# Kernel tuning notes

Hardware: AMD Instinct MI355X
Metric: run time of the kernel (lower is better)

The kernel has to match this reference:

```python
import jax, jax.numpy as jnp
import numpy as np

N_NODES = 50000
N_EDGES = 800000
D_IN = 128
D_OUT = 128


def setup_inputs() -> dict:
    key = jax.random.key(0)
    k1, k2, k3, k4, k5 = jax.random.split(key, 5)
    x = jax.random.normal(k1, (N_NODES, D_IN), dtype=jnp.float32)
    weight = jax.random.normal(k2, (D_IN, D_OUT), dtype=jnp.float32)
    bias = jax.random.normal(k3, (D_OUT,), dtype=jnp.float32)
    vals = jax.random.uniform(k4, (N_EDGES,), dtype=jnp.float32)
    row = jax.random.randint(k5, (N_EDGES,), 0, N_NODES, dtype=jnp.int32)
    col = jax.random.randint(jax.random.fold_in(k5, 1), (N_EDGES,), 0, N_NODES, dtype=jnp.int32)
    return {"x": x, "weight": weight, "bias": bias, "vals": vals, "row": row, "col": col}


def reference(x, weight, bias, vals, row, col):
    # Dense feature transform: x @ W   [N, D_out]
    h = x @ weight
    # SpMM: out[i] = sum_{e: row[e]==i} vals[e] * h[col[e]]
    msg = vals[:, None] * h[col]  # [E, D_out]
    out = jax.ops.segment_sum(msg, row, num_segments=N_NODES)
    # Fused bias + ReLU (original: out += bias; relu(out))
    out = jax.nn.relu(out + bias)
    return out
```

## Files before the change

kernel.cpp:

```cpp
#include <hip/hip_runtime.h>

#define N_NODES 50000
#define N_EDGES 800000
#define D 128
#define D4 32

#define BIN_LOG 6
#define BIN_ROWS 64
#define NBINS ((N_NODES + BIN_ROWS - 1) / BIN_ROWS)
#define CAP 1280

#define NKEYS 512

#define EPB 4096
#define NCHUNK ((N_EDGES + EPB - 1) / EPB)
#define GEMM_BLOCKS ((N_NODES + 63) / 64)
#define E4 (N_EDGES / 4)

#define CAP_CELL 24
#define CELLS_PER_BIN (NCHUNK * CAP_CELL)
#define CNTROW 784

typedef __attribute__((ext_vector_type(8))) short bf16x8;
typedef __attribute__((ext_vector_type(4))) float f32x4;

__device__ __forceinline__ unsigned bf16_1(float a) {
    unsigned u = __float_as_uint(a);
    return (u + 0x7fffu + ((u >> 16) & 1u)) >> 16;
}
__device__ __forceinline__ unsigned pack_bf16(float a, float b) {
    return bf16_1(a) | (bf16_1(b) << 16);
}
__device__ __forceinline__ float ubf_lo(unsigned u) {
    return __uint_as_float(u << 16);
}
__device__ __forceinline__ float ubf_hi(unsigned u) {
    return __uint_as_float(u & 0xffff0000u);
}

__global__ __launch_bounds__(256) void prep_wt(const float* __restrict__ w,
                                               unsigned* __restrict__ wtu) {
    const int i = blockIdx.x * 256 + threadIdx.x;
    if (i < D * 64) {
        const int col = i >> 6;
        const int k2  = i & 63;
        wtu[i] = pack_bf16(w[(size_t)(2 * k2) * D + col],
                           w[(size_t)(2 * k2 + 1) * D + col]);
    }
}

__global__ __launch_bounds__(256) void fused_partition_gemm(
        const float4* __restrict__ x4, const uint4* __restrict__ wt4,
        ushort* __restrict__ hb,
        const int4* __restrict__ rowi4, const int4* __restrict__ coli4,
        const float4* __restrict__ vals4,
        uint2* __restrict__ cells, ushort* __restrict__ cnt_t) {

    if (blockIdx.x < NCHUNK) {
        __shared__ int cur[NBINS];
        const int tid = threadIdx.x;
        for (int i = tid; i < NBINS; i += 256) cur[i] = 0;
        __syncthreads();

        union { int4 v4[4]; int a[16]; } R, C;
        union { float4 v4[4]; float a[16]; } V;
        const int base4 = blockIdx.x * (EPB / 4);
        #pragma unroll
        for (int q = 0; q < 4; ++q) {
            const int i4  = base4 + q * 256 + tid;
            const int i4c = (i4 < E4) ? i4 : (E4 - 1);
            R.v4[q] = rowi4[i4c];
            C.v4[q] = coli4[i4c];
            V.v4[q] = vals4[i4c];
            if (i4 >= E4) R.v4[q] = make_int4(-1, -1, -1, -1);
        }

        #pragma unroll
        for (int q = 0; q < 16; ++q) {
            const int r = R.a[q];
            if (r >= 0) {
                const int b = r >> BIN_LOG;
                const int k = atomicAdd(&cur[b], 1);
                const unsigned c = (unsigned)C.a[q];
                if (k < CAP_CELL)
                    cells[((size_t)b * NCHUNK + blockIdx.x) * CAP_CELL + k] =
                        make_uint2((c << 16) | bf16_1(V.a[q]),
                                   ((unsigned)(r & (BIN_ROWS - 1)) << 3) | (c >> 13));
            }
        }
        __syncthreads();

        ushort* ct = cnt_t + (size_t)blockIdx.x * CNTROW;
        for (int i = tid; i < NBINS; i += 256)
            ct[i] = (ushort)min(cur[i], CAP_CELL);
        return;
    }

    const int bid  = blockIdx.x - NCHUNK;
    const int lane = threadIdx.x & 63;
    const int r0   = bid * 64 + (threadIdx.x >> 6) * 16;
    const int arow = r0 + (lane & 15);
    const int kg   = lane >> 4;
    const bool rok = (arow < N_NODES);

    bf16x8 afr[4];
    #pragma unroll
    for (int kc = 0; kc < 4; ++kc) {
        float4 f0 = make_float4(0.f, 0.f, 0.f, 0.f);
        float4 f1 = f0;
        if (rok) {
            const int c4 = kc * 8 + kg * 2;
            f0 = x4[(size_t)arow * D4 + c4];
            f1 = x4[(size_t)arow * D4 + c4 + 1];
        }
        union { bf16x8 v; unsigned u[4]; } a;
        a.u[0] = pack_bf16(f0.x, f0.y);
        a.u[1] = pack_bf16(f0.z, f0.w);
        a.u[2] = pack_bf16(f1.x, f1.y);
        a.u[3] = pack_bf16(f1.z, f1.w);
        afr[kc] = a.v;
    }

    f32x4 acc[8];
    #pragma unroll
    for (int t = 0; t < 8; ++t) acc[t] = (f32x4){0.f, 0.f, 0.f, 0.f};

    #pragma unroll
    for (int t = 0; t < 8; ++t) {
        const int col = t * 16 + (lane & 15);
        #pragma unroll
        for (int kc = 0; kc < 4; ++kc) {
            union { bf16x8 v; uint4 u; } b;
            b.u = wt4[(size_t)col * 16 + kc * 4 + kg];
            acc[t] = __builtin_amdgcn_mfma_f32_16x16x32_bf16(afr[kc], b.v,
                                                             acc[t], 0, 0, 0);
        }
    }

    #pragma unroll
    for (int t = 0; t < 8; ++t) {
        const int col = t * 16 + (lane & 15);
        #pragma unroll
        for (int j = 0; j < 4; ++j) {
            const int r = r0 + (lane >> 4) * 4 + j;
            if (r < N_NODES)
                hb[(size_t)r * D + col] = (ushort)bf16_1(acc[t][j]);
        }
    }
}

__global__ __launch_bounds__(512) void sort_gather(const ushort* __restrict__ cnt_t,
                                                   const uint2* __restrict__ cells,
                                                   const uint2* __restrict__ hb2,
                                                   const float4* __restrict__ bias4,
                                                   float4* __restrict__ out4) {
    __shared__ ushort   cnt_c[NCHUNK];
    __shared__ int      hcnt[NKEYS];
    __shared__ int      cur[NKEYS];
    __shared__ int      starts[NKEYS + 1];
    __shared__ int      wsum[8], woff[8];
    __shared__ unsigned sorted[CAP];

    const int bin = blockIdx.x;
    const int tid = threadIdx.x;
    const uint2* stripe = cells + (size_t)bin * CELLS_PER_BIN;

    if (tid < NCHUNK) cnt_c[tid] = cnt_t[(size_t)tid * CNTROW + bin];
    if (tid < NKEYS) { hcnt[tid] = 0; cur[tid] = 0; }
    __syncthreads();

    for (int i = tid; i < CELLS_PER_BIN; i += 512) {
        const int c = i / CAP_CELL;
        const int s = i - c * CAP_CELL;
        if (s < (int)cnt_c[c])
            atomicAdd(&hcnt[stripe[i].y & (NKEYS - 1)], 1);
    }
    __syncthreads();

    {
        int v = hcnt[tid];
        #pragma unroll
        for (int off = 1; off < 64; off <<= 1) {
            const int t = __shfl_up(v, off);
            if ((tid & 63) >= off) v += t;
        }
        starts[tid + 1] = v;
        if ((tid & 63) == 63) wsum[tid >> 6] = v;
    }
    __syncthreads();
    if (tid == 0) {
        int run = 0;
        #pragma unroll
        for (int w2 = 0; w2 < 8; ++w2) { woff[w2] = run; run += wsum[w2]; }
        starts[0] = 0;
    }
    __syncthreads();
    starts[tid + 1] += woff[tid >> 6];
    __syncthreads();

    for (int i = tid; i < CELLS_PER_BIN; i += 512) {
        const int c = i / CAP_CELL;
        const int s = i - c * CAP_CELL;
        if (s < (int)cnt_c[c]) {
            const uint2 r = stripe[i];
            const int key = r.y & (NKEYS - 1);
            const int p = atomicAdd(&cur[key], 1);
            const int dst = starts[key] + p;
            if (dst < CAP) sorted[dst] = r.x;
        }
    }
    __syncthreads();

    const int wave = tid >> 6;
    const int lane = tid & 63;
    const int half = lane >> 5;
    const int hl   = lane & 31;
    const float4 b = bias4[hl];

    #pragma unroll
    for (int rp = 0; rp < 4; ++rp) {
        const int row  = wave + 16 * rp + 8 * half;
        const int node = bin * BIN_ROWS + row;
        int s = 0, len = 0;
        if (node < N_NODES) {
            s   = starts[row << 3];
            len = starts[(row << 3) + 8] - s;
        }
        int lm = len;
        lm = max(lm, __shfl_xor(lm, 32));

        float4 acc = {0.f, 0.f, 0.f, 0.f};
        for (int j0 = 0; j0 < lm; j0 += 8) {
            uint2 hv[8];
            float vv[8];
            #pragma unroll
            for (int q = 0; q < 8; ++q) {
                const int jq = j0 + q;
                const int jj = (jq < len) ? (s + jq) : 0;
                unsigned ed = sorted[jj];
                ed = (jq < len) ? ed : 0u;
                vv[q] = __uint_as_float((ed & 0xffffu) << 16);
                hv[q] = hb2[(size_t)(ed >> 16) * 32 + hl];
            }
            #pragma unroll
            for (int q = 0; q < 8; ++q) {
                acc.x = fmaf(vv[q], ubf_lo(hv[q].x), acc.x);
                acc.y = fmaf(vv[q], ubf_hi(hv[q].x), acc.y);
                acc.z = fmaf(vv[q], ubf_lo(hv[q].y), acc.z);
                acc.w = fmaf(vv[q], ubf_hi(hv[q].y), acc.w);
            }
        }
        if (node < N_NODES) {
            float4 o;
            o.x = fmaxf(acc.x + b.x, 0.f);
            o.y = fmaxf(acc.y + b.y, 0.f);
            o.z = fmaxf(acc.z + b.z, 0.f);
            o.w = fmaxf(acc.w + b.w, 0.f);
            out4[(size_t)node * 32 + hl] = o;
        }
    }
}

extern "C" void kernel_launch(void* const* d_in, const int* in_sizes, int n_in,
                              void* d_out, int out_size, void* d_ws, size_t ws_size,
                              hipStream_t stream) {
    const float* x      = (const float*)d_in[0];
    const float* weight = (const float*)d_in[1];
    const float* bias   = (const float*)d_in[2];
    const float* vals   = (const float*)d_in[3];
    const int*   rowi   = (const int*)d_in[4];
    const int*   coli   = (const int*)d_in[5];
    float* out = (float*)d_out;

    char* w = (char*)d_ws;
    ushort*   hb    = (ushort*)w;   w += (size_t)N_NODES * D * sizeof(ushort);
    unsigned* wt    = (unsigned*)w; w += (size_t)D * 64 * sizeof(unsigned);
    uint2*    cells = (uint2*)w;    w += (size_t)NBINS * CELLS_PER_BIN * sizeof(uint2);
    ushort*   cnt_t = (ushort*)w;

    prep_wt<<<32, 256, 0, stream>>>(weight, wt);

    fused_partition_gemm<<<NCHUNK + GEMM_BLOCKS, 256, 0, stream>>>(
        (const float4*)x, (const uint4*)wt, hb,
        (const int4*)rowi, (const int4*)coli, (const float4*)vals,
        cells, cnt_t);

    sort_gather<<<NBINS, 512, 0, stream>>>(cnt_t, cells, (const uint2*)hb,
                                           (const float4*)bias, (float4*)out);
}
```

Baseline: 79.46 us.

## Replace fixed-capacity per-chunk cells with counted, scanned compact bins

Adds a counting pass that builds a per-chunk bin histogram (fused with the weight prep) and a per-bin scan over chunks that produces exact write offsets. Edges are then placed contiguously into per-bin buffers instead of padded 24-slot cells. This lets the sort/gather kernel read only the real records instead of scanning every padded cell with divisions and count checks. In exchange, it adds one extra kernel launch and reads the row array a second time.

```diff
diff --git a/kernel.cpp b/kernel.cpp
--- a/kernel.cpp
+++ b/kernel.cpp
@@ -16,9 +16,6 @@
 #define NCHUNK ((N_EDGES + EPB - 1) / EPB)
 #define GEMM_BLOCKS ((N_NODES + 63) / 64)
 #define E4 (N_EDGES / 4)
-
-#define CAP_CELL 24
-#define CELLS_PER_BIN (NCHUNK * CAP_CELL)
 #define CNTROW 784
 
 typedef __attribute__((ext_vector_type(8))) short bf16x8;
@@ -38,28 +35,83 @@
     return __uint_as_float(u & 0xffff0000u);
 }
 
-__global__ __launch_bounds__(256) void prep_wt(const float* __restrict__ w,
-                                               unsigned* __restrict__ wtu) {
-    const int i = blockIdx.x * 256 + threadIdx.x;
-    if (i < D * 64) {
-        const int col = i >> 6;
-        const int k2  = i & 63;
-        wtu[i] = pack_bf16(w[(size_t)(2 * k2) * D + col],
-                           w[(size_t)(2 * k2 + 1) * D + col]);
-    }
-}
-
-__global__ __launch_bounds__(256) void fused_partition_gemm(
+__global__ __launch_bounds__(256) void count_and_prep(
+        const int4* __restrict__ rowi4, const float* __restrict__ w,
+        unsigned* __restrict__ wtu, ushort* __restrict__ cnt_t) {
+    if (blockIdx.x >= NCHUNK) {
+        const int i = (blockIdx.x - NCHUNK) * 256 + threadIdx.x;
+        if (i < D * 64) {
+            const int col = i >> 6;
+            const int k2  = i & 63;
+            wtu[i] = pack_bf16(w[(size_t)(2 * k2) * D + col],
+                               w[(size_t)(2 * k2 + 1) * D + col]);
+        }
+        return;
+    }
+
+    __shared__ int hist[NBINS];
+    const int tid = threadIdx.x;
+    for (int i = tid; i < NBINS; i += 256) hist[i] = 0;
+    __syncthreads();
+
+    #pragma unroll
+    for (int q = 0; q < 4; ++q) {
+        const int i4 = blockIdx.x * (EPB / 4) + q * 256 + tid;
+        if (i4 < E4) {
+            const int4 r = rowi4[i4];
+            atomicAdd(&hist[r.x >> BIN_LOG], 1);
+            atomicAdd(&hist[r.y >> BIN_LOG], 1);
+            atomicAdd(&hist[r.z >> BIN_LOG], 1);
+            atomicAdd(&hist[r.w >> BIN_LOG], 1);
+        }
+    }
+    __syncthreads();
+
+    ushort* ct = cnt_t + (size_t)blockIdx.x * CNTROW;
+    for (int i = tid; i < NBINS; i += 256) ct[i] = (ushort)hist[i];
+}
+
+__global__ __launch_bounds__(256) void scan_chunks(const ushort* __restrict__ cnt_t,
+                                                   ushort* __restrict__ base_t,
+                                                   int* __restrict__ total) {
+    __shared__ int wsum[4], woff[4];
+    const int bin = blockIdx.x;
+    const int tid = threadIdx.x;
+
+    int v = 0;
+    if (tid < NCHUNK) v = cnt_t[(size_t)tid * CNTROW + bin];
+    int incl = v;
+    #pragma unroll
+    for (int off = 1; off < 64; off <<= 1) {
+        const int t = __shfl_up(incl, off);
+        if ((tid & 63) >= off) incl += t;
+    }
+    if ((tid & 63) == 63) wsum[tid >> 6] = incl;
+    __syncthreads();
+    if (tid == 0) {
+        int run = 0;
+        #pragma unroll
+        for (int w2 = 0; w2 < 4; ++w2) { woff[w2] = run; run += wsum[w2]; }
+    }
+    __syncthreads();
+    incl += woff[tid >> 6];
+    if (tid < NCHUNK) base_t[(size_t)tid * CNTROW + bin] = (ushort)(incl - v);
+    if (tid == 255) total[bin] = incl;
+}
+
+__global__ __launch_bounds__(256) void place_and_gemm(
         const float4* __restrict__ x4, const uint4* __restrict__ wt4,
         ushort* __restrict__ hb,
         const int4* __restrict__ rowi4, const int4* __restrict__ coli4,
         const float4* __restrict__ vals4,
-        uint2* __restrict__ cells, ushort* __restrict__ cnt_t) {
+        const ushort* __restrict__ base_t, uint2* __restrict__ bins) {
 
     if (blockIdx.x < NCHUNK) {
+        __shared__ int sbase[NBINS];
         __shared__ int cur[NBINS];
         const int tid = threadIdx.x;
-        for (int i = tid; i < NBINS; i += 256) cur[i] = 0;
+        const ushort* br = base_t + (size_t)blockIdx.x * CNTROW;
+        for (int i = tid; i < NBINS; i += 256) { sbase[i] = br[i]; cur[i] = 0; }
         __syncthreads();
 
         union { int4 v4[4]; int a[16]; } R, C;
@@ -79,20 +131,15 @@
         for (int q = 0; q < 16; ++q) {
             const int r = R.a[q];
             if (r >= 0) {
-                const int b = r >> BIN_LOG;
-                const int k = atomicAdd(&cur[b], 1);
+                const int b   = r >> BIN_LOG;
+                const int pos = sbase[b] + atomicAdd(&cur[b], 1);
                 const unsigned c = (unsigned)C.a[q];
-                if (k < CAP_CELL)
-                    cells[((size_t)b * NCHUNK + blockIdx.x) * CAP_CELL + k] =
+                if (pos < CAP)
+                    bins[(size_t)b * CAP + pos] =
                         make_uint2((c << 16) | bf16_1(V.a[q]),
                                    ((unsigned)(r & (BIN_ROWS - 1)) << 3) | (c >> 13));
             }
         }
-        __syncthreads();
-
-        ushort* ct = cnt_t + (size_t)blockIdx.x * CNTROW;
-        for (int i = tid; i < NBINS; i += 256)
-            ct[i] = (ushort)min(cur[i], CAP_CELL);
         return;
     }
 
@@ -149,12 +196,11 @@
     }
 }
 
-__global__ __launch_bounds__(512) void sort_gather(const ushort* __restrict__ cnt_t,
-                                                   const uint2* __restrict__ cells,
+__global__ __launch_bounds__(512) void sort_gather(const int* __restrict__ total,
+                                                   const uint2* __restrict__ bins,
                                                    const uint2* __restrict__ hb2,
                                                    const float4* __restrict__ bias4,
                                                    float4* __restrict__ out4) {
-    __shared__ ushort   cnt_c[NCHUNK];
     __shared__ int      hcnt[NKEYS];
     __shared__ int      cur[NKEYS];
     __shared__ int      starts[NKEYS + 1];
@@ -163,18 +209,14 @@
 
     const int bin = blockIdx.x;
     const int tid = threadIdx.x;
-    const uint2* stripe = cells + (size_t)bin * CELLS_PER_BIN;
-
-    if (tid < NCHUNK) cnt_c[tid] = cnt_t[(size_t)tid * CNTROW + bin];
+    int n = total[bin];
+    n = (n > CAP) ? CAP : n;
+    const uint2* brec = bins + (size_t)bin * CAP;
+
     if (tid < NKEYS) { hcnt[tid] = 0; cur[tid] = 0; }
     __syncthreads();
 
-    for (int i = tid; i < CELLS_PER_BIN; i += 512) {
-        const int c = i / CAP_CELL;
-        const int s = i - c * CAP_CELL;
-        if (s < (int)cnt_c[c])
-            atomicAdd(&hcnt[stripe[i].y & (NKEYS - 1)], 1);
-    }
+    for (int i = tid; i < n; i += 512) atomicAdd(&hcnt[brec[i].y & (NKEYS - 1)], 1);
     __syncthreads();
 
     {
@@ -198,16 +240,12 @@
     starts[tid + 1] += woff[tid >> 6];
     __syncthreads();
 
-    for (int i = tid; i < CELLS_PER_BIN; i += 512) {
-        const int c = i / CAP_CELL;
-        const int s = i - c * CAP_CELL;
-        if (s < (int)cnt_c[c]) {
-            const uint2 r = stripe[i];
-            const int key = r.y & (NKEYS - 1);
-            const int p = atomicAdd(&cur[key], 1);
-            const int dst = starts[key] + p;
-            if (dst < CAP) sorted[dst] = r.x;
-        }
+    for (int i = tid; i < n; i += 512) {
+        const uint2 r = brec[i];
+        const int key = r.y & (NKEYS - 1);
+        const int p = atomicAdd(&cur[key], 1);
+        const int dst = starts[key] + p;
+        if (dst < CAP) sorted[dst] = r.x;
     }
     __syncthreads();
 
@@ -273,18 +311,23 @@
     float* out = (float*)d_out;
 
     char* w = (char*)d_ws;
-    ushort*   hb    = (ushort*)w;   w += (size_t)N_NODES * D * sizeof(ushort);
-    unsigned* wt    = (unsigned*)w; w += (size_t)D * 64 * sizeof(unsigned);
-    uint2*    cells = (uint2*)w;    w += (size_t)NBINS * CELLS_PER_BIN * sizeof(uint2);
-    ushort*   cnt_t = (ushort*)w;
-
-    prep_wt<<<32, 256, 0, stream>>>(weight, wt);
-
-    fused_partition_gemm<<<NCHUNK + GEMM_BLOCKS, 256, 0, stream>>>(
+    ushort*   hb     = (ushort*)w;   w += (size_t)N_NODES * D * sizeof(ushort);
+    unsigned* wt     = (unsigned*)w; w += (size_t)D * 64 * sizeof(unsigned);
+    ushort*   cnt_t  = (ushort*)w;   w += (size_t)NCHUNK * CNTROW * sizeof(ushort);
+    ushort*   base_t = (ushort*)w;   w += (size_t)NCHUNK * CNTROW * sizeof(ushort);
+    int*      total  = (int*)w;      w += ((size_t)NBINS + 16) * sizeof(int);
+    uint2*    bins   = (uint2*)w;
+
+    count_and_prep<<<NCHUNK + 32, 256, 0, stream>>>((const int4*)rowi, weight,
+                                                    wt, cnt_t);
+
+    scan_chunks<<<NBINS, 256, 0, stream>>>(cnt_t, base_t, total);
+
+    place_and_gemm<<<NCHUNK + GEMM_BLOCKS, 256, 0, stream>>>(
         (const float4*)x, (const uint4*)wt, hb,
         (const int4*)rowi, (const int4*)coli, (const float4*)vals,
-        cells, cnt_t);
-
-    sort_gather<<<NBINS, 512, 0, stream>>>(cnt_t, cells, (const uint2*)hb,
+        base_t, bins);
+
+    sort_gather<<<NBINS, 512, 0, stream>>>(total, bins, (const uint2*)hb,
                                            (const float4*)bias, (float4*)out);
 }
```

After: 71.56 us. -9.9%, faster.
